# Optimization experiments

Hardware: AMD Instinct MI355X
Metric: run time of the kernel (lower is better)

The kernel has to match this reference:

```python
import jax, jax.numpy as jnp
import numpy as np

B, N, D_IN = 4, 16384, 64          # batch, sequence (grid) length, model dim
H, DH = 8, 64                       # heads, dim per head
INNER = H * DH                      # 512


def setup_inputs() -> dict:
    key = jax.random.key(0)
    ks = jax.random.split(key, 7)
    s = 1.0 / np.sqrt(D_IN)
    return {
        "queries": jax.random.normal(ks[0], (B, N, D_IN), jnp.float32),
        "keys": jax.random.normal(ks[1], (B, N, D_IN), jnp.float32),
        "values": jax.random.normal(ks[2], (B, N, D_IN), jnp.float32),
        # torch nn.Linear weights are [out_features, in_features]
        "Wq": jax.random.normal(ks[3], (INNER, D_IN), jnp.float32) * s,
        "Wk": jax.random.normal(ks[4], (INNER, D_IN), jnp.float32) * s,
        "Wout": jax.random.normal(ks[5], (D_IN, INNER), jnp.float32) * (1.0 / np.sqrt(INNER)),
        "bout": jax.random.normal(ks[6], (D_IN,), jnp.float32) * 0.01,
    }


def reference(queries, keys, values, Wq, Wk, Wout, bout):
    b, n, _ = queries.shape
    # projections (NOTE: source uses to_k for values: values = self.to_k(values))
    q = (queries @ Wq.T).reshape(b, n, H, DH).transpose(0, 2, 1, 3)  # b h n d
    k = (keys    @ Wk.T).reshape(b, n, H, DH).transpose(0, 2, 1, 3)
    v = (values  @ Wk.T).reshape(b, n, H, DH).transpose(0, 2, 1, 3)
    # galerkin linear attention, associative form: (K^T V) first, then Q @ (.)
    # (the instance-norm outputs in the torch source are dead code on this path)
    dots = jnp.einsum('bhnd,bhne->bhde', k, v)            # [b,h,d,d]
    out = jnp.einsum('bhnd,bhde->bhne', q, dots) / n      # [b,h,n,d]
    out = out.transpose(0, 2, 1, 3).reshape(b, n, INNER)  # b n (h d)
    return out @ Wout.T + bout                             # [b,n,D_IN]
```

## Files before the change

kernel.cpp:

```cpp
#include <hip/hip_runtime.h>

#define NB 4
#define SEQ 16384
#define D 64
#define NH 8
#define INNER 512

typedef float f4 __attribute__((ext_vector_type(4)));

#define OFF_PART 0
#define OFF_S    (256 * 4096)
#define OFF_P    (OFF_S + NB * 4096)
#define OFF_Q    (OFF_P + 64 * INNER)
#define OFF_XT   (OFF_Q + INNER * D)
#define OFF_G    (OFF_XT + NB * 64 * INNER)

__global__ __launch_bounds__(256) void kA(const float* __restrict__ keys,
                                          const float* __restrict__ values,
                                          const float* __restrict__ Wq,
                                          const float* __restrict__ Wk,
                                          const float* __restrict__ Wout,
                                          float* __restrict__ ws) {
    const int bid = blockIdx.x;
    const int t = threadIdx.x;
    const int w = t >> 6, l = t & 63;
    const int dg = l >> 3, eg = l & 7;
    const int dbase = (w & 1) * 32 + dg * 4;
    const int ebase = (w >> 1) * 32 + eg * 4;

    f4 acc[4];
    #pragma unroll
    for (int a = 0; a < 4; ++a) acc[a] = (f4)0.f;

    if (bid < 256) {
        const int b = bid >> 6;
        const int row0 = (bid & 63) * 256;
        const float* kp = keys   + ((size_t)b * SEQ + row0) * D;
        const float* vp = values + ((size_t)b * SEQ + row0) * D;
        #pragma unroll 4
        for (int n = 0; n < 256; ++n) {
            f4 kv = *(const f4*)(kp + n * D + dbase);
            f4 vv = *(const f4*)(vp + n * D + ebase);
            #pragma unroll
            for (int a = 0; a < 4; ++a)
                acc[a] += kv[a] * vv;
        }
        float* pp = ws + OFF_PART + (size_t)bid * 4096;
        #pragma unroll
        for (int a = 0; a < 4; ++a)
            *(f4*)(pp + (dbase + a) * D + ebase) = acc[a];
    } else if (bid < 264) {
        const int h = bid - 256;
        const float* wqp = Wq + (size_t)h * 64 * D;
        const float* wkp = Wk + (size_t)h * 64 * D;
        #pragma unroll 4
        for (int i = 0; i < 64; ++i) {
            f4 a4 = *(const f4*)(wqp + i * D + dbase);
            f4 b4 = *(const f4*)(wkp + i * D + ebase);
            #pragma unroll
            for (int a = 0; a < 4; ++a)
                acc[a] += a4[a] * b4;
        }
        float* pp = ws + OFF_P;
        #pragma unroll
        for (int a = 0; a < 4; ++a)
            *(f4*)(pp + (dbase + a) * INNER + h * 64 + ebase) = acc[a];
    } else {
        const int h = bid - 264;
        const float* wkp = Wk + (size_t)h * 64 * D;
        #pragma unroll 2
        for (int iq = 0; iq < 16; ++iq) {
            f4 wo[4], wk4[4];
            #pragma unroll
            for (int a = 0; a < 4; ++a)
                wo[a] = *(const f4*)(Wout + (size_t)(dbase + a) * INNER + h * 64 + iq * 4);
            #pragma unroll
            for (int ii = 0; ii < 4; ++ii)
                wk4[ii] = *(const f4*)(wkp + (iq * 4 + ii) * D + ebase);
            #pragma unroll
            for (int a = 0; a < 4; ++a)
                #pragma unroll
                for (int ii = 0; ii < 4; ++ii)
                    acc[a] += wo[a][ii] * wk4[ii];
        }
        float* qp = ws + OFF_Q;
        #pragma unroll
        for (int a = 0; a < 4; ++a)
            *(f4*)(qp + (h * 64 + dbase + a) * D + ebase) = acc[a];
    }
}

__global__ __launch_bounds__(256) void kB(float* __restrict__ ws) {
    const int b = blockIdx.x >> 5;
    const int seg = blockIdx.x & 31;
    const int t = threadIdx.x;
    const int el = seg * 128 + (t & 127);
    const int half = t >> 7;
    const float* pp = ws + OFF_PART + (size_t)b * 64 * 4096 + el;
    float s = 0.f;
    #pragma unroll 8
    for (int p = 0; p < 32; ++p)
        s += pp[(size_t)(half * 32 + p) * 4096];
    __shared__ float red[256];
    red[t] = s;
    __syncthreads();
    if (t < 128)
        ws[OFF_S + b * 4096 + el] = red[t] + red[t + 128];
}

__global__ __launch_bounds__(256) void kC(float* __restrict__ ws) {
    const int b = blockIdx.x >> 3, h = blockIdx.x & 7;
    const int t = threadIdx.x;
    if (h == 0) {
        f4 z = (f4)0.f;
        #pragma unroll
        for (int m = 0; m < 4; ++m)
            *(f4*)(ws + OFF_G + b * 4096 + t * 16 + m * 4) = z;
    }
    const int w = t >> 6, l = t & 63;
    const int dbase = (w & 1) * 32 + (l >> 3) * 4;
    const int ebase = (w >> 1) * 32 + (l & 7) * 4;
    const float* Sp = ws + OFF_S + b * 4096;
    const float* Qp = ws + OFF_Q + h * 64 * D;
    float acc[4][4];
    #pragma unroll
    for (int a = 0; a < 4; ++a)
        #pragma unroll
        for (int c = 0; c < 4; ++c) acc[a][c] = 0.f;
    #pragma unroll 2
    for (int iq = 0; iq < 16; ++iq) {
        f4 s4[4], q4[4];
        #pragma unroll
        for (int a = 0; a < 4; ++a) s4[a] = *(const f4*)(Sp + (dbase + a) * D + iq * 4);
        #pragma unroll
        for (int c = 0; c < 4; ++c) q4[c] = *(const f4*)(Qp + (ebase + c) * D + iq * 4);
        #pragma unroll
        for (int a = 0; a < 4; ++a)
            #pragma unroll
            for (int c = 0; c < 4; ++c)
                #pragma unroll
                for (int ii = 0; ii < 4; ++ii)
                    acc[a][c] = fmaf(s4[a][ii], q4[c][ii], acc[a][c]);
    }
    float* xp = ws + OFF_XT + (size_t)b * 64 * INNER;
    #pragma unroll
    for (int c = 0; c < 4; ++c) {
        f4 o;
        o[0] = acc[0][c]; o[1] = acc[1][c]; o[2] = acc[2][c]; o[3] = acc[3][c];
        *(f4*)(xp + (size_t)(ebase + c) * INNER + h * 64 + dbase) = o;
    }
}

__global__ __launch_bounds__(256) void kD(float* __restrict__ ws) {
    const int b = blockIdx.x >> 4;
    const int kc = (blockIdx.x & 15) * 32;
    const int t = threadIdx.x;
    const int w = t >> 6, l = t & 63;
    const int dbase = (w & 1) * 32 + (l >> 3) * 4;
    const int ebase = (w >> 1) * 32 + (l & 7) * 4;
    const float* Pp = ws + OFF_P;
    const float* Xp = ws + OFF_XT + (size_t)b * 64 * INNER;
    float acc[4][4];
    #pragma unroll
    for (int a = 0; a < 4; ++a)
        #pragma unroll
        for (int c = 0; c < 4; ++c) acc[a][c] = 0.f;
    #pragma unroll
    for (int kq = 0; kq < 8; ++kq) {
        f4 p4[4], x4[4];
        #pragma unroll
        for (int a = 0; a < 4; ++a) p4[a] = *(const f4*)(Pp + (size_t)(dbase + a) * INNER + kc + kq * 4);
        #pragma unroll
        for (int c = 0; c < 4; ++c) x4[c] = *(const f4*)(Xp + (size_t)(ebase + c) * INNER + kc + kq * 4);
        #pragma unroll
        for (int a = 0; a < 4; ++a)
            #pragma unroll
            for (int c = 0; c < 4; ++c)
                #pragma unroll
                for (int ii = 0; ii < 4; ++ii)
                    acc[a][c] = fmaf(p4[a][ii], x4[c][ii], acc[a][c]);
    }
    const float invn = 1.0f / (float)SEQ;
    float* Gp = ws + OFF_G + b * 4096;
    #pragma unroll
    for (int a = 0; a < 4; ++a)
        #pragma unroll
        for (int c = 0; c < 4; ++c)
            atomicAdd(&Gp[(dbase + a) * D + ebase + c], acc[a][c] * invn);
}

__global__ __launch_bounds__(256) void kE(const float* __restrict__ queries,
                                          const float* __restrict__ bout,
                                          const float* __restrict__ ws,
                                          float* __restrict__ out) {
    __shared__ float GTs[4096];
    const int bid = blockIdx.x;
    const int b = bid >> 6;
    const int row0 = (bid & 63) * 256;
    const int t = threadIdx.x;
    {
        const int d = t >> 2;
        const int e0 = (t & 3) * 16;
        #pragma unroll
        for (int m4 = 0; m4 < 4; ++m4) {
            f4 g = *(const f4*)(ws + OFF_G + b * 4096 + d * 64 + e0 + m4 * 4);
            #pragma unroll
            for (int mm = 0; mm < 4; ++mm) {
                const int e = e0 + m4 * 4 + mm;
                GTs[e * 64 + (((d >> 2) ^ ((e >> 3) & 7)) << 2) + (d & 3)] = g[mm];
            }
        }
    }
    __syncthreads();

    const int w = t >> 6, l = t & 63;
    const int ng = l >> 3, eg = l & 7;
    const f4 bo0 = *(const f4*)(bout + eg * 8);
    const f4 bo1 = *(const f4*)(bout + eg * 8 + 4);
    const float* qp = queries + ((size_t)b * SEQ + row0 + w * 64) * D;
    float* op = out + ((size_t)b * SEQ + row0 + w * 64) * D;

    #pragma unroll
    for (int sub = 0; sub < 2; ++sub) {
        const float* qs = qp + (sub * 32 + ng * 4) * D;
        f4 acc[4][2];
        #pragma unroll
        for (int r = 0; r < 4; ++r) { acc[r][0] = (f4)0.f; acc[r][1] = (f4)0.f; }
        #pragma unroll 4
        for (int dq = 0; dq < 16; ++dq) {
            f4 q4[4], g4[8];
            #pragma unroll
            for (int r = 0; r < 4; ++r)
                q4[r] = *(const f4*)(qs + r * D + dq * 4);
            #pragma unroll
            for (int c = 0; c < 8; ++c) {
                const int e = eg * 8 + c;
                g4[c] = *(const f4*)&GTs[e * 64 + ((dq ^ eg) << 2)];
            }
            #pragma unroll
            for (int r = 0; r < 4; ++r)
                #pragma unroll
                for (int c = 0; c < 8; ++c)
                    #pragma unroll
                    for (int ii = 0; ii < 4; ++ii)
                        acc[r][c >> 2][c & 3] = fmaf(q4[r][ii], g4[c][ii], acc[r][c >> 2][c & 3]);
        }
        #pragma unroll
        for (int r = 0; r < 4; ++r) {
            const int row = (sub * 32 + ng * 4 + r) * D;
            f4 o0 = acc[r][0] + bo0;
            f4 o1 = acc[r][1] + bo1;
            *(f4*)(op + row + eg * 8) = o0;
            *(f4*)(op + row + eg * 8 + 4) = o1;
        }
    }
}

extern "C" void kernel_launch(void* const* d_in, const int* in_sizes, int n_in,
                              void* d_out, int out_size, void* d_ws, size_t ws_size,
                              hipStream_t stream) {
    const float* queries = (const float*)d_in[0];
    const float* keys    = (const float*)d_in[1];
    const float* values  = (const float*)d_in[2];
    const float* Wq      = (const float*)d_in[3];
    const float* Wk      = (const float*)d_in[4];
    const float* Wout    = (const float*)d_in[5];
    const float* bout    = (const float*)d_in[6];
    float* ws = (float*)d_ws;

    kA<<<272, 256, 0, stream>>>(keys, values, Wq, Wk, Wout, ws);
    kB<<<128, 256, 0, stream>>>(ws);
    kC<<<32,  256, 0, stream>>>(ws);
    kD<<<64,  256, 0, stream>>>(ws);
    kE<<<256, 256, 0, stream>>>(queries, bout, ws, (float*)d_out);
}
```

Before: 158.4 us.

## Restructure pipeline: atomic S reduction, per-batch weight folding, finer-grained grids

Replaces the five-kernel pipeline with a memset plus four kernels. The K^T V partials are now accumulated with atomics over 1024 smaller blocks, which removes the separate partial-sum reduction pass. The weight folding is reordered to compute Wk·S·Wk^T per (batch, head) and then Wq·U·Wout, producing the transposed G directly. The output kernel now reads G from global memory instead of staging it in LDS and uses 1024 smaller blocks. Together this trims launches and workspace traffic, at the cost of more atomic contention and global rather than LDS reads of G in the main kernel.

```diff
diff --git a/kernel.cpp b/kernel.cpp
--- a/kernel.cpp
+++ b/kernel.cpp
@@ -8,251 +8,214 @@
 
 typedef float f4 __attribute__((ext_vector_type(4)));
 
-#define OFF_PART 0
-#define OFF_S    (256 * 4096)
-#define OFF_P    (OFF_S + NB * 4096)
-#define OFF_Q    (OFF_P + 64 * INNER)
-#define OFF_XT   (OFF_Q + INNER * D)
-#define OFF_G    (OFF_XT + NB * 64 * INNER)
+#define OFF_S  0
+#define OFF_GT (NB * 4096)
+#define OFF_U  (2 * NB * 4096)
 
 __global__ __launch_bounds__(256) void kA(const float* __restrict__ keys,
                                           const float* __restrict__ values,
-                                          const float* __restrict__ Wq,
-                                          const float* __restrict__ Wk,
-                                          const float* __restrict__ Wout,
-                                          float* __restrict__ ws) {
+                                          float* __restrict__ S) {
     const int bid = blockIdx.x;
-    const int t = threadIdx.x;
-    const int w = t >> 6, l = t & 63;
-    const int dg = l >> 3, eg = l & 7;
-    const int dbase = (w & 1) * 32 + dg * 4;
-    const int ebase = (w >> 1) * 32 + eg * 4;
-
+    const int b = bid >> 8;
+    const int row0 = (bid & 255) * 64;
+    const int t = threadIdx.x;
+    const int di = t >> 4, ej = t & 15;
+    const float* kp = keys   + ((size_t)b * SEQ + row0) * D + di * 4;
+    const float* vp = values + ((size_t)b * SEQ + row0) * D + ej * 4;
     f4 acc[4];
     #pragma unroll
-    for (int a = 0; a < 4; ++a) acc[a] = (f4)0.f;
-
-    if (bid < 256) {
-        const int b = bid >> 6;
-        const int row0 = (bid & 63) * 256;
-        const float* kp = keys   + ((size_t)b * SEQ + row0) * D;
-        const float* vp = values + ((size_t)b * SEQ + row0) * D;
-        #pragma unroll 4
-        for (int n = 0; n < 256; ++n) {
-            f4 kv = *(const f4*)(kp + n * D + dbase);
-            f4 vv = *(const f4*)(vp + n * D + ebase);
-            #pragma unroll
-            for (int a = 0; a < 4; ++a)
-                acc[a] += kv[a] * vv;
+    for (int r = 0; r < 4; ++r) acc[r] = (f4)0.f;
+    #pragma unroll 8
+    for (int n = 0; n < 64; ++n) {
+        f4 k4 = *(const f4*)(kp + n * D);
+        f4 v4 = *(const f4*)(vp + n * D);
+        #pragma unroll
+        for (int r = 0; r < 4; ++r)
+            acc[r] += k4[r] * v4;
+    }
+    float* Sb = S + b * 4096;
+    #pragma unroll
+    for (int r = 0; r < 4; ++r)
+        #pragma unroll
+        for (int c = 0; c < 4; ++c)
+            atomicAdd(&Sb[(di * 4 + r) * 64 + ej * 4 + c], acc[r][c]);
+}
+
+__global__ __launch_bounds__(256) void kC1(const float* __restrict__ Wk,
+                                           float* __restrict__ ws) {
+    __shared__ float T[64 * 65];
+    const int b = blockIdx.x >> 3, h = blockIdx.x & 7;
+    const int t = threadIdx.x;
+    const int di = t >> 4, ej = t & 15;
+    const float* Sb  = ws + OFF_S + b * 4096;
+    const float* Wkh = Wk + (size_t)h * 64 * D;
+
+    f4 acc[4];
+    #pragma unroll
+    for (int r = 0; r < 4; ++r) acc[r] = (f4)0.f;
+    for (int j4 = 0; j4 < 16; ++j4) {
+        f4 ak[4], bs[4];
+        #pragma unroll
+        for (int r = 0; r < 4; ++r)  ak[r] = *(const f4*)(Wkh + (di * 4 + r) * D + j4 * 4);
+        #pragma unroll
+        for (int jj = 0; jj < 4; ++jj) bs[jj] = *(const f4*)(Sb + (j4 * 4 + jj) * D + ej * 4);
+        #pragma unroll
+        for (int r = 0; r < 4; ++r)
+            #pragma unroll
+            for (int jj = 0; jj < 4; ++jj)
+                acc[r] += ak[r][jj] * bs[jj];
+    }
+    #pragma unroll
+    for (int r = 0; r < 4; ++r)
+        #pragma unroll
+        for (int c = 0; c < 4; ++c)
+            T[(di * 4 + r) * 65 + ej * 4 + ((c + di) & 3)] = acc[r][c];
+    __syncthreads();
+
+    float a2[4][4];
+    #pragma unroll
+    for (int r = 0; r < 4; ++r)
+        #pragma unroll
+        for (int c = 0; c < 4; ++c) a2[r][c] = 0.f;
+    for (int i4 = 0; i4 < 16; ++i4) {
+        float av[4][4];
+        f4 bw[4];
+        #pragma unroll
+        for (int ii = 0; ii < 4; ++ii)
+            #pragma unroll
+            for (int r = 0; r < 4; ++r)
+                av[r][ii] = T[(di * 4 + r) * 65 + i4 * 4 + ((ii + di) & 3)];
+        #pragma unroll
+        for (int c = 0; c < 4; ++c)
+            bw[c] = *(const f4*)(Wkh + (ej * 4 + c) * D + i4 * 4);
+        #pragma unroll
+        for (int r = 0; r < 4; ++r)
+            #pragma unroll
+            for (int c = 0; c < 4; ++c)
+                #pragma unroll
+                for (int ii = 0; ii < 4; ++ii)
+                    a2[r][c] = fmaf(av[r][ii], bw[c][ii], a2[r][c]);
+    }
+    float* Up = ws + OFF_U + (size_t)(b * 8 + h) * 4096;
+    #pragma unroll
+    for (int r = 0; r < 4; ++r) {
+        f4 o; o[0] = a2[r][0]; o[1] = a2[r][1]; o[2] = a2[r][2]; o[3] = a2[r][3];
+        *(f4*)(Up + (di * 4 + r) * 64 + ej * 4) = o;
+    }
+}
+
+__global__ __launch_bounds__(256) void kC2(const float* __restrict__ Wq,
+                                           const float* __restrict__ Wout,
+                                           float* __restrict__ ws) {
+    __shared__ float T[64 * 65];
+    const int b = blockIdx.x >> 3, h = blockIdx.x & 7;
+    const int t = threadIdx.x;
+    const int di = t >> 4, ej = t & 15;
+    const float* Up = ws + OFF_U + (size_t)(b * 8 + h) * 4096;
+
+    float acc[4][4];
+    #pragma unroll
+    for (int r = 0; r < 4; ++r)
+        #pragma unroll
+        for (int c = 0; c < 4; ++c) acc[r][c] = 0.f;
+    for (int i4 = 0; i4 < 16; ++i4) {
+        f4 wq4[4], bu[4];
+        #pragma unroll
+        for (int ii = 0; ii < 4; ++ii) {
+            wq4[ii] = *(const f4*)(Wq + (size_t)(64 * h + i4 * 4 + ii) * D + di * 4);
+            bu[ii]  = *(const f4*)(Up + (i4 * 4 + ii) * 64 + ej * 4);
         }
-        float* pp = ws + OFF_PART + (size_t)bid * 4096;
-        #pragma unroll
-        for (int a = 0; a < 4; ++a)
-            *(f4*)(pp + (dbase + a) * D + ebase) = acc[a];
-    } else if (bid < 264) {
-        const int h = bid - 256;
-        const float* wqp = Wq + (size_t)h * 64 * D;
-        const float* wkp = Wk + (size_t)h * 64 * D;
-        #pragma unroll 4
-        for (int i = 0; i < 64; ++i) {
-            f4 a4 = *(const f4*)(wqp + i * D + dbase);
-            f4 b4 = *(const f4*)(wkp + i * D + ebase);
-            #pragma unroll
-            for (int a = 0; a < 4; ++a)
-                acc[a] += a4[a] * b4;
-        }
-        float* pp = ws + OFF_P;
-        #pragma unroll
-        for (int a = 0; a < 4; ++a)
-            *(f4*)(pp + (dbase + a) * INNER + h * 64 + ebase) = acc[a];
-    } else {
-        const int h = bid - 264;
-        const float* wkp = Wk + (size_t)h * 64 * D;
-        #pragma unroll 2
-        for (int iq = 0; iq < 16; ++iq) {
-            f4 wo[4], wk4[4];
-            #pragma unroll
-            for (int a = 0; a < 4; ++a)
-                wo[a] = *(const f4*)(Wout + (size_t)(dbase + a) * INNER + h * 64 + iq * 4);
-            #pragma unroll
-            for (int ii = 0; ii < 4; ++ii)
-                wk4[ii] = *(const f4*)(wkp + (iq * 4 + ii) * D + ebase);
-            #pragma unroll
-            for (int a = 0; a < 4; ++a)
-                #pragma unroll
-                for (int ii = 0; ii < 4; ++ii)
-                    acc[a] += wo[a][ii] * wk4[ii];
-        }
-        float* qp = ws + OFF_Q;
-        #pragma unroll
-        for (int a = 0; a < 4; ++a)
-            *(f4*)(qp + (h * 64 + dbase + a) * D + ebase) = acc[a];
-    }
-}
-
-__global__ __launch_bounds__(256) void kB(float* __restrict__ ws) {
-    const int b = blockIdx.x >> 5;
-    const int seg = blockIdx.x & 31;
-    const int t = threadIdx.x;
-    const int el = seg * 128 + (t & 127);
-    const int half = t >> 7;
-    const float* pp = ws + OFF_PART + (size_t)b * 64 * 4096 + el;
-    float s = 0.f;
-    #pragma unroll 8
-    for (int p = 0; p < 32; ++p)
-        s += pp[(size_t)(half * 32 + p) * 4096];
-    __shared__ float red[256];
-    red[t] = s;
+        #pragma unroll
+        for (int r = 0; r < 4; ++r)
+            #pragma unroll
+            for (int c = 0; c < 4; ++c)
+                #pragma unroll
+                for (int ii = 0; ii < 4; ++ii)
+                    acc[r][c] = fmaf(wq4[ii][r], bu[ii][c], acc[r][c]);
+    }
+    #pragma unroll
+    for (int r = 0; r < 4; ++r)
+        #pragma unroll
+        for (int c = 0; c < 4; ++c)
+            T[(di * 4 + r) * 65 + ej * 4 + ((c + di) & 3)] = acc[r][c];
     __syncthreads();
-    if (t < 128)
-        ws[OFF_S + b * 4096 + el] = red[t] + red[t + 128];
-}
-
-__global__ __launch_bounds__(256) void kC(float* __restrict__ ws) {
-    const int b = blockIdx.x >> 3, h = blockIdx.x & 7;
-    const int t = threadIdx.x;
-    if (h == 0) {
-        f4 z = (f4)0.f;
-        #pragma unroll
-        for (int m = 0; m < 4; ++m)
-            *(f4*)(ws + OFF_G + b * 4096 + t * 16 + m * 4) = z;
-    }
-    const int w = t >> 6, l = t & 63;
-    const int dbase = (w & 1) * 32 + (l >> 3) * 4;
-    const int ebase = (w >> 1) * 32 + (l & 7) * 4;
-    const float* Sp = ws + OFF_S + b * 4096;
-    const float* Qp = ws + OFF_Q + h * 64 * D;
-    float acc[4][4];
-    #pragma unroll
-    for (int a = 0; a < 4; ++a)
-        #pragma unroll
-        for (int c = 0; c < 4; ++c) acc[a][c] = 0.f;
-    #pragma unroll 2
-    for (int iq = 0; iq < 16; ++iq) {
-        f4 s4[4], q4[4];
-        #pragma unroll
-        for (int a = 0; a < 4; ++a) s4[a] = *(const f4*)(Sp + (dbase + a) * D + iq * 4);
-        #pragma unroll
-        for (int c = 0; c < 4; ++c) q4[c] = *(const f4*)(Qp + (ebase + c) * D + iq * 4);
-        #pragma unroll
-        for (int a = 0; a < 4; ++a)
-            #pragma unroll
-            for (int c = 0; c < 4; ++c)
-                #pragma unroll
-                for (int ii = 0; ii < 4; ++ii)
-                    acc[a][c] = fmaf(s4[a][ii], q4[c][ii], acc[a][c]);
-    }
-    float* xp = ws + OFF_XT + (size_t)b * 64 * INNER;
-    #pragma unroll
-    for (int c = 0; c < 4; ++c) {
-        f4 o;
-        o[0] = acc[0][c]; o[1] = acc[1][c]; o[2] = acc[2][c]; o[3] = acc[3][c];
-        *(f4*)(xp + (size_t)(ebase + c) * INNER + h * 64 + dbase) = o;
-    }
-}
-
-__global__ __launch_bounds__(256) void kD(float* __restrict__ ws) {
-    const int b = blockIdx.x >> 4;
-    const int kc = (blockIdx.x & 15) * 32;
-    const int t = threadIdx.x;
-    const int w = t >> 6, l = t & 63;
-    const int dbase = (w & 1) * 32 + (l >> 3) * 4;
-    const int ebase = (w >> 1) * 32 + (l & 7) * 4;
-    const float* Pp = ws + OFF_P;
-    const float* Xp = ws + OFF_XT + (size_t)b * 64 * INNER;
-    float acc[4][4];
-    #pragma unroll
-    for (int a = 0; a < 4; ++a)
-        #pragma unroll
-        for (int c = 0; c < 4; ++c) acc[a][c] = 0.f;
-    #pragma unroll
-    for (int kq = 0; kq < 8; ++kq) {
-        f4 p4[4], x4[4];
-        #pragma unroll
-        for (int a = 0; a < 4; ++a) p4[a] = *(const f4*)(Pp + (size_t)(dbase + a) * INNER + kc + kq * 4);
-        #pragma unroll
-        for (int c = 0; c < 4; ++c) x4[c] = *(const f4*)(Xp + (size_t)(ebase + c) * INNER + kc + kq * 4);
-        #pragma unroll
-        for (int a = 0; a < 4; ++a)
-            #pragma unroll
-            for (int c = 0; c < 4; ++c)
-                #pragma unroll
-                for (int ii = 0; ii < 4; ++ii)
-                    acc[a][c] = fmaf(p4[a][ii], x4[c][ii], acc[a][c]);
+
+    float a2[4][4];
+    #pragma unroll
+    for (int r = 0; r < 4; ++r)
+        #pragma unroll
+        for (int c = 0; c < 4; ++c) a2[r][c] = 0.f;
+    for (int i4 = 0; i4 < 16; ++i4) {
+        float av[4][4];
+        f4 bw[4];
+        #pragma unroll
+        for (int ii = 0; ii < 4; ++ii)
+            #pragma unroll
+            for (int r = 0; r < 4; ++r)
+                av[r][ii] = T[(di * 4 + r) * 65 + i4 * 4 + ((ii + di) & 3)];
+        #pragma unroll
+        for (int c = 0; c < 4; ++c)
+            bw[c] = *(const f4*)(Wout + (size_t)(ej * 4 + c) * INNER + 64 * h + i4 * 4);
+        #pragma unroll
+        for (int r = 0; r < 4; ++r)
+            #pragma unroll
+            for (int c = 0; c < 4; ++c)
+                #pragma unroll
+                for (int ii = 0; ii < 4; ++ii)
+                    a2[r][c] = fmaf(av[r][ii], bw[c][ii], a2[r][c]);
     }
     const float invn = 1.0f / (float)SEQ;
-    float* Gp = ws + OFF_G + b * 4096;
-    #pragma unroll
-    for (int a = 0; a < 4; ++a)
-        #pragma unroll
-        for (int c = 0; c < 4; ++c)
-            atomicAdd(&Gp[(dbase + a) * D + ebase + c], acc[a][c] * invn);
+    float* GTb = ws + OFF_GT + b * 4096;
+    #pragma unroll
+    for (int r = 0; r < 4; ++r)
+        #pragma unroll
+        for (int c = 0; c < 4; ++c)
+            atomicAdd(&GTb[(ej * 4 + c) * 64 + di * 4 + r], a2[r][c] * invn);
 }
 
 __global__ __launch_bounds__(256) void kE(const float* __restrict__ queries,
                                           const float* __restrict__ bout,
                                           const float* __restrict__ ws,
                                           float* __restrict__ out) {
-    __shared__ float GTs[4096];
     const int bid = blockIdx.x;
-    const int b = bid >> 6;
-    const int row0 = (bid & 63) * 256;
-    const int t = threadIdx.x;
-    {
-        const int d = t >> 2;
-        const int e0 = (t & 3) * 16;
-        #pragma unroll
-        for (int m4 = 0; m4 < 4; ++m4) {
-            f4 g = *(const f4*)(ws + OFF_G + b * 4096 + d * 64 + e0 + m4 * 4);
-            #pragma unroll
-            for (int mm = 0; mm < 4; ++mm) {
-                const int e = e0 + m4 * 4 + mm;
-                GTs[e * 64 + (((d >> 2) ^ ((e >> 3) & 7)) << 2) + (d & 3)] = g[mm];
-            }
-        }
-    }
-    __syncthreads();
-
+    const int b = bid >> 8;
+    const int row0 = (bid & 255) * 64;
+    const int t = threadIdx.x;
     const int w = t >> 6, l = t & 63;
-    const int ng = l >> 3, eg = l & 7;
-    const f4 bo0 = *(const f4*)(bout + eg * 8);
-    const f4 bo1 = *(const f4*)(bout + eg * 8 + 4);
-    const float* qp = queries + ((size_t)b * SEQ + row0 + w * 64) * D;
-    float* op = out + ((size_t)b * SEQ + row0 + w * 64) * D;
-
-    #pragma unroll
-    for (int sub = 0; sub < 2; ++sub) {
-        const float* qs = qp + (sub * 32 + ng * 4) * D;
-        f4 acc[4][2];
-        #pragma unroll
-        for (int r = 0; r < 4; ++r) { acc[r][0] = (f4)0.f; acc[r][1] = (f4)0.f; }
-        #pragma unroll 4
-        for (int dq = 0; dq < 16; ++dq) {
-            f4 q4[4], g4[8];
-            #pragma unroll
-            for (int r = 0; r < 4; ++r)
-                q4[r] = *(const f4*)(qs + r * D + dq * 4);
-            #pragma unroll
-            for (int c = 0; c < 8; ++c) {
-                const int e = eg * 8 + c;
-                g4[c] = *(const f4*)&GTs[e * 64 + ((dq ^ eg) << 2)];
-            }
-            #pragma unroll
-            for (int r = 0; r < 4; ++r)
-                #pragma unroll
-                for (int c = 0; c < 8; ++c)
-                    #pragma unroll
-                    for (int ii = 0; ii < 4; ++ii)
-                        acc[r][c >> 2][c & 3] = fmaf(q4[r][ii], g4[c][ii], acc[r][c >> 2][c & 3]);
-        }
-        #pragma unroll
-        for (int r = 0; r < 4; ++r) {
-            const int row = (sub * 32 + ng * 4 + r) * D;
-            f4 o0 = acc[r][0] + bo0;
-            f4 o1 = acc[r][1] + bo1;
-            *(f4*)(op + row + eg * 8) = o0;
-            *(f4*)(op + row + eg * 8 + 4) = o1;
-        }
+    const int rg = l >> 4, eg = l & 15;
+    const float* GT = ws + OFF_GT + b * 4096;
+    const size_t rbase = (size_t)b * SEQ + row0 + w * 16 + rg * 4;
+    const float* qp = queries + rbase * D;
+    float acc[4][4];
+    #pragma unroll
+    for (int r = 0; r < 4; ++r)
+        #pragma unroll
+        for (int c = 0; c < 4; ++c) acc[r][c] = 0.f;
+    #pragma unroll 2
+    for (int dq = 0; dq < 16; ++dq) {
+        f4 q4[4], g4[4];
+        #pragma unroll
+        for (int r = 0; r < 4; ++r)
+            q4[r] = *(const f4*)(qp + r * D + dq * 4);
+        #pragma unroll
+        for (int c = 0; c < 4; ++c)
+            g4[c] = *(const f4*)(GT + (eg * 4 + c) * 64 + dq * 4);
+        #pragma unroll
+        for (int r = 0; r < 4; ++r)
+            #pragma unroll
+            for (int c = 0; c < 4; ++c)
+                #pragma unroll
+                for (int ii = 0; ii < 4; ++ii)
+                    acc[r][c] = fmaf(q4[r][ii], g4[c][ii], acc[r][c]);
+    }
+    const f4 bo = *(const f4*)(bout + eg * 4);
+    float* op = out + rbase * D;
+    #pragma unroll
+    for (int r = 0; r < 4; ++r) {
+        f4 o;
+        o[0] = acc[r][0] + bo[0]; o[1] = acc[r][1] + bo[1];
+        o[2] = acc[r][2] + bo[2]; o[3] = acc[r][3] + bo[3];
+        *(f4*)(op + r * D + eg * 4) = o;
     }
 }
 
@@ -268,9 +231,10 @@
     const float* bout    = (const float*)d_in[6];
     float* ws = (float*)d_ws;
 
-    kA<<<272, 256, 0, stream>>>(keys, values, Wq, Wk, Wout, ws);
-    kB<<<128, 256, 0, stream>>>(ws);
-    kC<<<32,  256, 0, stream>>>(ws);
-    kD<<<64,  256, 0, stream>>>(ws);
-    kE<<<256, 256, 0, stream>>>(queries, bout, ws, (float*)d_out);
-}
+    hipMemsetAsync(ws, 0, (size_t)2 * NB * 4096 * sizeof(float), stream);
+
+    kA <<<1024, 256, 0, stream>>>(keys, values, ws + OFF_S);
+    kC1<<<32,   256, 0, stream>>>(Wk, ws);
+    kC2<<<32,   256, 0, stream>>>(Wq, Wout, ws);
+    kE <<<1024, 256, 0, stream>>>(queries, bout, ws, (float*)d_out);
+}
```

Result: slower. 234.4 us (+48.0%).
